# Performance work log

Hardware: AMD Instinct MI355X
Metric: run time of the kernel (lower is better)

The kernel has to match this reference:

```python
import jax, jax.numpy as jnp
import numpy as np

W_DIM, T_DIM = 300, 100
IN = W_DIM + T_DIM        # 400, also LSTM hidden size
H = IN                    # hiddenSize
BI = 2 * H                # 800, biLSTM output per step
MLP_IN = 2 * BI           # 1600
VOCAB, NTAGS = 50000, 50
SEQ = 320


def _lstm_dir(xs, w_ih, w_hh, b_ih, b_hh, h0, c0, reverse):
    # xs: [T, d_in]; PyTorch gate order i, f, g, o
    if reverse:
        xs = xs[::-1]
    def step(carry, x):
        h, c = carry
        g = x @ w_ih.T + h @ w_hh.T + b_ih + b_hh
        i, f, gc, o = jnp.split(g, 4)
        i, f, o = jax.nn.sigmoid(i), jax.nn.sigmoid(f), jax.nn.sigmoid(o)
        c = f * c + i * jnp.tanh(gc)
        h = o * jnp.tanh(c)
        return (h, c), h
    _, ys = jax.lax.scan(step, (h0, c0), xs)
    return ys[::-1] if reverse else ys


def _bilstm(x, params, h0, c0):
    # x: [T, IN]; h0/c0: [4, H] ordered (l0 fwd, l0 bwd, l1 fwd, l1 bwd)
    out = x
    for layer in range(2):
        p_f = params[layer][0]
        p_b = params[layer][1]
        yf = _lstm_dir(out, *p_f, h0[2 * layer],     c0[2 * layer],     False)
        yb = _lstm_dir(out, *p_b, h0[2 * layer + 1], c0[2 * layer + 1], True)
        out = jnp.concatenate([yf, yb], axis=-1)  # [T, 2H]
    return out


def setup_inputs() -> dict:
    key = jax.random.key(0)
    ks = iter(jax.random.split(key, 32))
    inp = {}
    inp['words'] = jax.random.randint(next(ks), (SEQ,), 0, VOCAB)
    inp['tags'] = jax.random.randint(next(ks), (SEQ,), 0, NTAGS)
    inp['arcs'] = jax.random.randint(next(ks), (SEQ + 1,), 0, SEQ + 1)
    inp['word_emb'] = jax.random.normal(next(ks), (VOCAB, W_DIM), jnp.float32) * 0.1
    inp['tag_emb'] = jax.random.normal(next(ks), (NTAGS, T_DIM), jnp.float32) * 0.1
    inp['h0'] = jax.random.normal(next(ks), (4, H), jnp.float32)
    inp['c0'] = jax.random.normal(next(ks), (4, H), jnp.float32)
    s = 1.0 / np.sqrt(H)
    for layer, d_in in ((0, IN), (1, BI)):
        for suf in ('', 'r'):
            inp[f'w_ih_l{layer}{suf}'] = jax.random.uniform(next(ks), (4 * H, d_in), jnp.float32, -s, s)
            inp[f'w_hh_l{layer}{suf}'] = jax.random.uniform(next(ks), (4 * H, H), jnp.float32, -s, s)
            inp[f'b_ih_l{layer}{suf}'] = jax.random.uniform(next(ks), (4 * H,), jnp.float32, -s, s)
            inp[f'b_hh_l{layer}{suf}'] = jax.random.uniform(next(ks), (4 * H,), jnp.float32, -s, s)
    inp['mlp_w1'] = jax.random.normal(next(ks), (MLP_IN, MLP_IN), jnp.float32) * 0.02
    inp['mlp_b1'] = jnp.zeros((MLP_IN,), jnp.float32)
    inp['mlp_w2'] = jax.random.normal(next(ks), (1, MLP_IN), jnp.float32) * 0.02
    inp['mlp_b2'] = jnp.zeros((1,), jnp.float32)
    return inp


def reference(words, tags, arcs, word_emb, tag_emb, h0, c0,
              w_ih_l0, w_hh_l0, b_ih_l0, b_hh_l0,
              w_ih_l0r, w_hh_l0r, b_ih_l0r, b_hh_l0r,
              w_ih_l1, w_hh_l1, b_ih_l1, b_hh_l1,
              w_ih_l1r, w_hh_l1r, b_ih_l1r, b_hh_l1r,
              mlp_w1, mlp_b1, mlp_w2, mlp_b2):
    n = words.shape[0]
    x = jnp.concatenate([word_emb[words], tag_emb[tags]], axis=1)  # [n, IN]
    params = (((w_ih_l0, w_hh_l0, b_ih_l0, b_hh_l0), (w_ih_l0r, w_hh_l0r, b_ih_l0r, b_hh_l0r)),
              ((w_ih_l1, w_hh_l1, b_ih_l1, b_hh_l1), (w_ih_l1r, w_hh_l1r, b_ih_l1r, b_hh_l1r)))
    hv = _bilstm(x, params, h0, c0)  # [n, BI]
    # pairwise MLP: concat(h_head, h_dep) @ W1.T == h_head @ W1a.T + h_dep @ W1b.T
    w1a, w1b = mlp_w1[:, :BI], mlp_w1[:, BI:]
    a = hv @ w1a.T  # [n, MLP_IN], head part
    b = hv @ w1b.T  # [n, MLP_IN], dep part
    hid = jax.nn.relu(a[:, None, :] + b[None, :, :] + mlp_b1)  # [n, n, MLP_IN]
    scores = jnp.einsum('ndk,ok->nd', hid, mlp_w2)[..., 0] if mlp_w2.shape[0] != 1 else (hid @ mlp_w2[0] + mlp_b2[0])  # [n, n]
    offdiag = 1.0 - jnp.eye(n, dtype=scores.dtype)
    score_tensor = jnp.zeros((n + 1, n + 1), scores.dtype)
    score_tensor = score_tensor.at[0, 0].set(1.0)
    score_tensor = score_tensor.at[1:, 1:].set(scores * offdiag)
    return score_tensor
```

## Files before the change

### kernel.cpp

```cpp
#include <hip/hip_runtime.h>
#include <hip/hip_bf16.h>
#include <hip/hip_fp16.h>

#define SEQ   320
#define HDIM  400
#define GATES 1600
#define NCOL  3200
#define GDW   16
#define RPW   25

typedef _Float16 half2v __attribute__((ext_vector_type(2)));
typedef _Float16 f16x8  __attribute__((ext_vector_type(8)));
typedef float    f32x4  __attribute__((ext_vector_type(4)));
union H2U { unsigned u; half2v h; __half2 hh; };

__global__ __launch_bounds__(256) void embed_f16_kernel(
    const int* __restrict__ words, const int* __restrict__ tags,
    const float* __restrict__ wemb, const float* __restrict__ temb,
    _Float16* __restrict__ xh)
{
    int i = blockIdx.x * 256 + threadIdx.x;
    if (i >= SEQ * 416) return;
    int t = i / 416, c = i % 416;
    float v = 0.f;
    if (c < 300)      v = wemb[(size_t)words[t] * 300 + c];
    else if (c < 400) v = temb[(size_t)tags[t] * 100 + (c - 300)];
    xh[i] = (_Float16)v;
}

__global__ __launch_bounds__(256) void cvtB_kernel(
    const float* __restrict__ B0, const float* __restrict__ B1, int ldb,
    int K, int Kp, _Float16* __restrict__ dst)
{
    int i = blockIdx.x * 256 + threadIdx.x;
    if (i >= NCOL * Kp) return;
    int n = i / Kp, k = i % Kp;
    float v = 0.f;
    if (k < K)
        v = (n < GATES) ? B0[(size_t)n * ldb + k] : B1[(size_t)(n - GATES) * ldb + k];
    dst[i] = (_Float16)v;
}

__global__ __launch_bounds__(256) void cvtA_kernel(
    const float* __restrict__ src, _Float16* __restrict__ dst, int n)
{
    int i = blockIdx.x * 256 + threadIdx.x;
    if (i < n) dst[i] = (_Float16)src[i];
}

__global__ __launch_bounds__(256) void bias_kernel(
    const float* __restrict__ bihl0,  const float* __restrict__ bhhl0,
    const float* __restrict__ bihl0r, const float* __restrict__ bhhl0r,
    const float* __restrict__ bihl1,  const float* __restrict__ bhhl1,
    const float* __restrict__ bihl1r, const float* __restrict__ bhhl1r,
    const float* __restrict__ mlpb1,
    float* __restrict__ bL0, float* __restrict__ bL1, float* __restrict__ bAB)
{
    int g = blockIdx.x * 256 + threadIdx.x;
    if (g >= NCOL) return;
    if (g < GATES) {
        bL0[g] = bihl0[g] + bhhl0[g];
        bL1[g] = bihl1[g] + bhhl1[g];
        bAB[g] = mlpb1[g];
    } else {
        int q = g - GATES;
        bL0[g] = bihl0r[q] + bhhl0r[q];
        bL1[g] = bihl1r[q] + bhhl1r[q];
        bAB[g] = 0.f;
    }
}

__global__ __launch_bounds__(256) void gemm_f16(
    const _Float16* __restrict__ A, int Kp,
    const _Float16* __restrict__ B,
    const float* __restrict__ bias, float* __restrict__ C)
{
    const int tid  = threadIdx.x;
    const int w    = tid >> 6, lane = tid & 63;
    const int quad = lane >> 4, l16 = lane & 15;
    const int mb   = blockIdx.y * 32 + (w & 1) * 16;
    const int n0   = blockIdx.x * 64 + (w >> 1) * 32;
    const _Float16* Arow = A + (size_t)(mb + l16) * Kp + quad * 8;
    const _Float16* B0r  = B + (size_t)(n0 + l16) * Kp + quad * 8;
    const _Float16* B1r  = B0r + (size_t)16 * Kp;
    f32x4 acc0 = {0.f, 0.f, 0.f, 0.f}, acc1 = {0.f, 0.f, 0.f, 0.f};
#pragma unroll 4
    for (int k0 = 0; k0 < Kp; k0 += 32) {
        f16x8 a  = *(const f16x8*)(Arow + k0);
        f16x8 b0 = *(const f16x8*)(B0r + k0);
        f16x8 b1 = *(const f16x8*)(B1r + k0);
        acc0 = __builtin_amdgcn_mfma_f32_16x16x32_f16(a, b0, acc0, 0, 0, 0);
        acc1 = __builtin_amdgcn_mfma_f32_16x16x32_f16(a, b1, acc1, 0, 0, 0);
    }
    const int mr = mb + quad * 4;
    float bn0 = bias[n0 + l16], bn1 = bias[n0 + 16 + l16];
#pragma unroll
    for (int r = 0; r < 4; ++r) {
        C[(size_t)(mr + r) * NCOL + n0 + l16]      = acc0[r] + bn0;
        C[(size_t)(mr + r) * NCOL + n0 + 16 + l16] = acc1[r] + bn1;
    }
}

__global__ __launch_bounds__(1024, 4) void lstm_layer(
    const float* __restrict__ gates,
    const float* __restrict__ whh_f, const float* __restrict__ whh_b,
    const float* __restrict__ h0f, const float* __restrict__ h0b,
    const float* __restrict__ c0f, const float* __restrict__ c0b,
    float* out)
{
    __shared__ unsigned h_pk[200];
    __shared__ float part[16][28];
    const int tid = threadIdx.x;
    const int dir = blockIdx.x >> 4;
    const int wg  = blockIdx.x & 15;
    const int j0  = wg * RPW;
    const float* whh = dir ? whh_b : whh_f;
    const float* h0d = dir ? h0b : h0f;
    const float* c0d = dir ? c0b : c0f;

    const int w    = tid >> 6;
    const int lane = tid & 63;
    const int g    = w & 3;
    const int kq   = w >> 2;
    const int half = lane & 1;
    const int r    = lane >> 1;
    const int jrow = j0 + (r < RPW ? r : RPW - 1);

    unsigned wr[26];
    {
        const float2* wp = (const float2*)(whh + (size_t)(g * 400 + jrow) * 400 +
                                           kq * 100 + 48 * half);
#pragma unroll
        for (int i = 0; i < 26; ++i) {
            H2U cv; float2 f = wp[i];
            cv.hh = __floats2half2_rn(f.x, f.y);
            wr[i] = (half == 0 && i >= 24) ? 0u : cv.u;
        }
    }

    const int pc = tid % 100;
    const int pr = tid / 100;
    float c_prev = (tid < RPW) ? c0d[j0 + tid] : 0.f;

    for (int s = 0; s < 320; ++s) {
        const int row = dir ? (319 - s) : s;

        float gv0 = 0.f, gv1 = 0.f, gv2 = 0.f, gv3 = 0.f;
        if (tid < RPW) {
            const float* gx = gates + (size_t)row * NCOL + dir * GATES + j0 + tid;
            gv0 = gx[0]; gv1 = gx[400]; gv2 = gx[800]; gv3 = gx[1200];
        }

        if (s == 0) {
            if (tid < 100) {
                float4 f = ((const float4*)h0d)[tid];
                H2U a, b;
                a.hh = __floats2half2_rn(f.x, f.y);
                b.hh = __floats2half2_rn(f.z, f.w);
                ((uint2*)h_pk)[tid] = make_uint2(a.u, b.u);
            }
        } else if (pr < 4) {
            const int rp = dir ? (row + 1) : (row - 1);
            const unsigned long long* src =
                (const unsigned long long*)(out + (size_t)rp * 800 + dir * 400) + pc * 2;
            unsigned long long a, b;
            for (;;) {
                a = __hip_atomic_load(src,     __ATOMIC_RELAXED, __HIP_MEMORY_SCOPE_AGENT);
                b = __hip_atomic_load(src + 1, __ATOMIC_RELAXED, __HIP_MEMORY_SCOPE_AGENT);
                if ((unsigned)a != 0xFFFFFFFFu && (unsigned)(a >> 32) != 0xFFFFFFFFu &&
                    (unsigned)b != 0xFFFFFFFFu && (unsigned)(b >> 32) != 0xFFFFFFFFu)
                    break;
            }
            H2U p0, p1;
            p0.hh = __floats2half2_rn(__uint_as_float((unsigned)a),
                                      __uint_as_float((unsigned)(a >> 32)));
            p1.hh = __floats2half2_rn(__uint_as_float((unsigned)b),
                                      __uint_as_float((unsigned)(b >> 32)));
            ((uint2*)h_pk)[pc] = make_uint2(p0.u, p1.u);
        }
        __syncthreads();

        {
            const uint2* hp2 = (const uint2*)h_pk + kq * 25 + 12 * half;
            float acc = 0.f;
#pragma unroll
            for (int i = 0; i < 13; ++i) {
                uint2 hv = hp2[i];
                H2U w0, w1, x0, x1;
                w0.u = wr[2 * i]; w1.u = wr[2 * i + 1];
                x0.u = hv.x;      x1.u = hv.y;
                acc = __builtin_amdgcn_fdot2(w0.h, x0.h, acc, false);
                acc = __builtin_amdgcn_fdot2(w1.h, x1.h, acc, false);
            }
            acc += __shfl_xor(acc, 1, 64);
            if (half == 0 && r < RPW) part[w][r] = acc;
        }
        __syncthreads();

        if (tid < RPW) {
            float gi = gv0 + ((part[0][tid] + part[4][tid]) + (part[8][tid]  + part[12][tid]));
            float gf = gv1 + ((part[1][tid] + part[5][tid]) + (part[9][tid]  + part[13][tid]));
            float gg = gv2 + ((part[2][tid] + part[6][tid]) + (part[10][tid] + part[14][tid]));
            float go = gv3 + ((part[3][tid] + part[7][tid]) + (part[11][tid] + part[15][tid]));
            float iv = 1.f / (1.f + __expf(-gi));
            float fv = 1.f / (1.f + __expf(-gf));
            float ov = 1.f / (1.f + __expf(-go));
            float tg = 1.f - 2.f / (1.f + __expf(2.f * gg));
            c_prev = fv * c_prev + iv * tg;
            float tc = 1.f - 2.f / (1.f + __expf(2.f * c_prev));
            float hv = ov * tc;
            __hip_atomic_store((unsigned*)(out + (size_t)row * 800 + dir * 400 + j0 + tid),
                               __float_as_uint(hv), __ATOMIC_RELAXED,
                               __HIP_MEMORY_SCOPE_AGENT);
        }
    }
}

__global__ __launch_bounds__(256) void scores_kernel(
    const float* __restrict__ ab, const float* __restrict__ w2,
    const float* __restrict__ b2, float* __restrict__ out)
{
    __shared__ float a_s[16 * 132];
    __shared__ float b_s[16 * 132];
    __shared__ float w_s[128];
    const int tx = threadIdx.x, ty = threadIdx.y;
    const int tid = ty * 16 + tx;
    const int n0 = blockIdx.y * 16, d0 = blockIdx.x * 16;
    float acc = 0.f;
    for (int kc = 0; kc < 1600; kc += 128) {
        for (int i = tid; i < 16 * 128; i += 256) {
            int r = i >> 7, c = i & 127;
            a_s[r * 132 + c] = ab[(size_t)(n0 + r) * NCOL + kc + c];
            b_s[r * 132 + c] = ab[(size_t)(d0 + r) * NCOL + 1600 + kc + c];
        }
        if (tid < 128) w_s[tid] = w2[kc + tid];
        __syncthreads();
#pragma unroll
        for (int k = 0; k < 128; k += 4) {
            float4 av = *(const float4*)&a_s[ty * 132 + k];
            float4 bv = *(const float4*)&b_s[tx * 132 + k];
            float4 wv = *(const float4*)&w_s[k];
            acc += fmaxf(av.x + bv.x, 0.f) * wv.x;
            acc += fmaxf(av.y + bv.y, 0.f) * wv.y;
            acc += fmaxf(av.z + bv.z, 0.f) * wv.z;
            acc += fmaxf(av.w + bv.w, 0.f) * wv.w;
        }
        __syncthreads();
    }
    int n = n0 + ty, d = d0 + tx;
    out[(size_t)(n + 1) * 321 + (d + 1)] = (n == d) ? 0.f : (acc + b2[0]);
}

__global__ void border_kernel(float* out) {
    int i = blockIdx.x * 256 + threadIdx.x;
    if (i < 321) {
        out[i]               = (i == 0) ? 1.f : 0.f;
        out[(size_t)i * 321] = (i == 0) ? 1.f : 0.f;
    }
}

extern "C" void kernel_launch(void* const* d_in, const int* in_sizes, int n_in,
                              void* d_out, int out_size, void* d_ws, size_t ws_size,
                              hipStream_t stream)
{
    const int*   words    = (const int*)d_in[0];
    const int*   tags     = (const int*)d_in[1];
    const float* wemb     = (const float*)d_in[3];
    const float* temb     = (const float*)d_in[4];
    const float* h0       = (const float*)d_in[5];
    const float* c0       = (const float*)d_in[6];
    const float* w_ih_l0  = (const float*)d_in[7];
    const float* w_hh_l0  = (const float*)d_in[8];
    const float* b_ih_l0  = (const float*)d_in[9];
    const float* b_hh_l0  = (const float*)d_in[10];
    const float* w_ih_l0r = (const float*)d_in[11];
    const float* w_hh_l0r = (const float*)d_in[12];
    const float* b_ih_l0r = (const float*)d_in[13];
    const float* b_hh_l0r = (const float*)d_in[14];
    const float* w_ih_l1  = (const float*)d_in[15];
    const float* w_hh_l1  = (const float*)d_in[16];
    const float* b_ih_l1  = (const float*)d_in[17];
    const float* b_hh_l1  = (const float*)d_in[18];
    const float* w_ih_l1r = (const float*)d_in[19];
    const float* w_hh_l1r = (const float*)d_in[20];
    const float* b_ih_l1r = (const float*)d_in[21];
    const float* b_hh_l1r = (const float*)d_in[22];
    const float* mlp_w1   = (const float*)d_in[23];
    const float* mlp_b1   = (const float*)d_in[24];
    const float* mlp_w2   = (const float*)d_in[25];
    const float* mlp_b2   = (const float*)d_in[26];
    float* out = (float*)d_out;

    float* ws     = (float*)d_ws;
    float* out0   = ws + 128000;
    float* out1   = ws + 384000;
    float* gates  = ws + 640000;
    float* biasL0 = ws + 1664000;
    float* biasL1 = ws + 1667200;
    float* biasAB = ws + 1670400;
    _Float16* Ah  = (_Float16*)(ws + 1673600);
    _Float16* Bh  = (_Float16*)(ws + 1801600);

    hipMemsetAsync(out0, 0xFF, (size_t)2 * 256000 * 4, stream);

    embed_f16_kernel<<<520, 256, 0, stream>>>(words, tags, wemb, temb, Ah);
    bias_kernel<<<13, 256, 0, stream>>>(b_ih_l0, b_hh_l0, b_ih_l0r, b_hh_l0r,
                                        b_ih_l1, b_hh_l1, b_ih_l1r, b_hh_l1r,
                                        mlp_b1, biasL0, biasL1, biasAB);

    cvtB_kernel<<<(NCOL * 416 + 255) / 256, 256, 0, stream>>>(
        w_ih_l0, w_ih_l0r, 400, 400, 416, Bh);
    gemm_f16<<<dim3(50, 10), 256, 0, stream>>>(Ah, 416, Bh, biasL0, gates);
    lstm_layer<<<2 * GDW, 1024, 0, stream>>>(gates, w_hh_l0, w_hh_l0r,
                                             h0, h0 + 400, c0, c0 + 400, out0);

    cvtA_kernel<<<1000, 256, 0, stream>>>(out0, Ah, 256000);
    cvtB_kernel<<<(NCOL * 800 + 255) / 256, 256, 0, stream>>>(
        w_ih_l1, w_ih_l1r, 800, 800, 800, Bh);
    gemm_f16<<<dim3(50, 10), 256, 0, stream>>>(Ah, 800, Bh, biasL1, gates);
    lstm_layer<<<2 * GDW, 1024, 0, stream>>>(gates, w_hh_l1, w_hh_l1r,
                                             h0 + 800, h0 + 1200, c0 + 800, c0 + 1200,
                                             out1);

    cvtA_kernel<<<1000, 256, 0, stream>>>(out1, Ah, 256000);
    cvtB_kernel<<<(NCOL * 800 + 255) / 256, 256, 0, stream>>>(
        mlp_w1, mlp_w1 + 800, 1600, 800, 800, Bh);
    gemm_f16<<<dim3(50, 10), 256, 0, stream>>>(Ah, 800, Bh, biasAB, gates);

    dim3 sgrid(20, 20), sblock(16, 16);
    scores_kernel<<<sgrid, sblock, 0, stream>>>(gates, mlp_w2, mlp_b2, out);
    border_kernel<<<2, 256, 0, stream>>>(out);
}
```

Baseline: 1.582 ms.

## Exchange packed fp16 hidden state between LSTM workgroups and fuse prep kernels

```diff
diff --git a/kernel.cpp b/kernel.cpp
--- a/kernel.cpp
+++ b/kernel.cpp
@@ -3,7 +3,6 @@
 #include <hip/hip_fp16.h>
 
 #define SEQ   320
-#define HDIM  400
 #define GATES 1600
 #define NCOL  3200
 #define GDW   16
@@ -14,59 +13,71 @@
 typedef float    f32x4  __attribute__((ext_vector_type(4)));
 union H2U { unsigned u; half2v h; __half2 hh; };
 
-__global__ __launch_bounds__(256) void embed_f16_kernel(
+__global__ __launch_bounds__(256) void prep_kernel(
     const int* __restrict__ words, const int* __restrict__ tags,
     const float* __restrict__ wemb, const float* __restrict__ temb,
-    _Float16* __restrict__ xh)
-{
-    int i = blockIdx.x * 256 + threadIdx.x;
-    if (i >= SEQ * 416) return;
-    int t = i / 416, c = i % 416;
-    float v = 0.f;
-    if (c < 300)      v = wemb[(size_t)words[t] * 300 + c];
-    else if (c < 400) v = temb[(size_t)tags[t] * 100 + (c - 300)];
-    xh[i] = (_Float16)v;
-}
-
-__global__ __launch_bounds__(256) void cvtB_kernel(
-    const float* __restrict__ B0, const float* __restrict__ B1, int ldb,
-    int K, int Kp, _Float16* __restrict__ dst)
-{
-    int i = blockIdx.x * 256 + threadIdx.x;
-    if (i >= NCOL * Kp) return;
-    int n = i / Kp, k = i % Kp;
-    float v = 0.f;
-    if (k < K)
-        v = (n < GATES) ? B0[(size_t)n * ldb + k] : B1[(size_t)(n - GATES) * ldb + k];
-    dst[i] = (_Float16)v;
-}
-
-__global__ __launch_bounds__(256) void cvtA_kernel(
-    const float* __restrict__ src, _Float16* __restrict__ dst, int n)
-{
-    int i = blockIdx.x * 256 + threadIdx.x;
-    if (i < n) dst[i] = (_Float16)src[i];
-}
-
-__global__ __launch_bounds__(256) void bias_kernel(
+    _Float16* __restrict__ Ah0,
     const float* __restrict__ bihl0,  const float* __restrict__ bhhl0,
     const float* __restrict__ bihl0r, const float* __restrict__ bhhl0r,
     const float* __restrict__ bihl1,  const float* __restrict__ bhhl1,
     const float* __restrict__ bihl1r, const float* __restrict__ bhhl1r,
     const float* __restrict__ mlpb1,
-    float* __restrict__ bL0, float* __restrict__ bL1, float* __restrict__ bAB)
-{
-    int g = blockIdx.x * 256 + threadIdx.x;
-    if (g >= NCOL) return;
-    if (g < GATES) {
-        bL0[g] = bihl0[g] + bhhl0[g];
-        bL1[g] = bihl1[g] + bhhl1[g];
-        bAB[g] = mlpb1[g];
+    float* __restrict__ bL0, float* __restrict__ bL1, float* __restrict__ bAB,
+    const float* __restrict__ wih0, const float* __restrict__ wih0r,
+    _Float16* __restrict__ BhA)
+{
+    const int b = blockIdx.x, t = threadIdx.x;
+    if (b < 520) {
+        int i = b * 256 + t;
+        if (i >= SEQ * 416) return;
+        int tt = i / 416, c = i % 416;
+        float v = 0.f;
+        if (c < 300)      v = wemb[(size_t)words[tt] * 300 + c];
+        else if (c < 400) v = temb[(size_t)tags[tt] * 100 + (c - 300)];
+        Ah0[i] = (_Float16)v;
+    } else if (b < 533) {
+        int g = (b - 520) * 256 + t;
+        if (g >= NCOL) return;
+        if (g < GATES) {
+            bL0[g] = bihl0[g] + bhhl0[g];
+            bL1[g] = bihl1[g] + bhhl1[g];
+            bAB[g] = mlpb1[g];
+        } else {
+            int q = g - GATES;
+            bL0[g] = bihl0r[q] + bhhl0r[q];
+            bL1[g] = bihl1r[q] + bhhl1r[q];
+            bAB[g] = 0.f;
+        }
     } else {
-        int q = g - GATES;
-        bL0[g] = bihl0r[q] + bhhl0r[q];
-        bL1[g] = bihl1r[q] + bhhl1r[q];
-        bAB[g] = 0.f;
+        int i = (b - 533) * 256 + t;
+        if (i >= NCOL * 416) return;
+        int n = i / 416, k = i % 416;
+        float v = 0.f;
+        if (k < 400)
+            v = (n < GATES) ? wih0[(size_t)n * 400 + k]
+                            : wih0r[(size_t)(n - GATES) * 400 + k];
+        BhA[i] = (_Float16)v;
+    }
+}
+
+__global__ __launch_bounds__(256) void cvt2_kernel(
+    const float* __restrict__ wih1, const float* __restrict__ wih1r,
+    _Float16* __restrict__ BhB,
+    const float* __restrict__ mlpw1, _Float16* __restrict__ BhA)
+{
+    const int b = blockIdx.x, t = threadIdx.x;
+    if (b < 10000) {
+        int i = b * 256 + t;
+        if (i >= NCOL * 800) return;
+        int n = i / 800, k = i % 800;
+        BhB[i] = (_Float16)((n < GATES) ? wih1[(size_t)n * 800 + k]
+                                        : wih1r[(size_t)(n - GATES) * 800 + k]);
+    } else {
+        int i = (b - 10000) * 256 + t;
+        if (i >= NCOL * 800) return;
+        int n = i / 800, k = i % 800;
+        BhA[i] = (_Float16)((n < GATES) ? mlpw1[(size_t)n * 1600 + k]
+                                        : mlpw1[(size_t)(n - GATES) * 1600 + 800 + k]);
     }
 }
 
@@ -106,10 +117,12 @@
     const float* __restrict__ whh_f, const float* __restrict__ whh_b,
     const float* __restrict__ h0f, const float* __restrict__ h0b,
     const float* __restrict__ c0f, const float* __restrict__ c0b,
-    float* out)
+    unsigned* __restrict__ ex,
+    _Float16* __restrict__ ah)
 {
     __shared__ unsigned h_pk[200];
     __shared__ float part[16][28];
+    unsigned short* hs = (unsigned short*)h_pk;
     const int tid = threadIdx.x;
     const int dir = blockIdx.x >> 4;
     const int wg  = blockIdx.x & 15;
@@ -138,8 +151,8 @@
         }
     }
 
-    const int pc = tid % 100;
-    const int pr = tid / 100;
+    const int pp = tid / 13;
+    const int pd = tid - pp * 13;
     float c_prev = (tid < RPW) ? c0d[j0 + tid] : 0.f;
 
     for (int s = 0; s < 320; ++s) {
@@ -159,24 +172,18 @@
                 b.hh = __floats2half2_rn(f.z, f.w);
                 ((uint2*)h_pk)[tid] = make_uint2(a.u, b.u);
             }
-        } else if (pr < 4) {
+        } else if (tid < 208 && pp != wg) {
             const int rp = dir ? (row + 1) : (row - 1);
-            const unsigned long long* src =
-                (const unsigned long long*)(out + (size_t)rp * 800 + dir * 400) + pc * 2;
-            unsigned long long a, b;
+            const unsigned* src = ex + (((size_t)dir * GDW + pp) * SEQ + rp) * 16 + pd;
+            unsigned v;
             for (;;) {
-                a = __hip_atomic_load(src,     __ATOMIC_RELAXED, __HIP_MEMORY_SCOPE_AGENT);
-                b = __hip_atomic_load(src + 1, __ATOMIC_RELAXED, __HIP_MEMORY_SCOPE_AGENT);
-                if ((unsigned)a != 0xFFFFFFFFu && (unsigned)(a >> 32) != 0xFFFFFFFFu &&
-                    (unsigned)b != 0xFFFFFFFFu && (unsigned)(b >> 32) != 0xFFFFFFFFu)
-                    break;
-            }
-            H2U p0, p1;
-            p0.hh = __floats2half2_rn(__uint_as_float((unsigned)a),
-                                      __uint_as_float((unsigned)(a >> 32)));
-            p1.hh = __floats2half2_rn(__uint_as_float((unsigned)b),
-                                      __uint_as_float((unsigned)(b >> 32)));
-            ((uint2*)h_pk)[pc] = make_uint2(p0.u, p1.u);
+                v = __hip_atomic_load(src, __ATOMIC_RELAXED, __HIP_MEMORY_SCOPE_AGENT);
+                if ((v & 0xFFFFu) != 0xFFFFu &&
+                    (pd == 12 || (v >> 16) != 0xFFFFu)) break;
+            }
+            const int hb = pp * RPW + pd * 2;
+            hs[hb] = (unsigned short)(v & 0xFFFFu);
+            if (pd < 12) hs[hb + 1] = (unsigned short)(v >> 16);
         }
         __syncthreads();
 
@@ -185,10 +192,10 @@
             float acc = 0.f;
 #pragma unroll
             for (int i = 0; i < 13; ++i) {
-                uint2 hv = hp2[i];
+                uint2 hv2 = hp2[i];
                 H2U w0, w1, x0, x1;
                 w0.u = wr[2 * i]; w1.u = wr[2 * i + 1];
-                x0.u = hv.x;      x1.u = hv.y;
+                x0.u = hv2.x;     x1.u = hv2.y;
                 acc = __builtin_amdgcn_fdot2(w0.h, x0.h, acc, false);
                 acc = __builtin_amdgcn_fdot2(w1.h, x1.h, acc, false);
             }
@@ -197,6 +204,7 @@
         }
         __syncthreads();
 
+        float hv = 0.f;
         if (tid < RPW) {
             float gi = gv0 + ((part[0][tid] + part[4][tid]) + (part[8][tid]  + part[12][tid]));
             float gf = gv1 + ((part[1][tid] + part[5][tid]) + (part[9][tid]  + part[13][tid]));
@@ -208,10 +216,24 @@
             float tg = 1.f - 2.f / (1.f + __expf(2.f * gg));
             c_prev = fv * c_prev + iv * tg;
             float tc = 1.f - 2.f / (1.f + __expf(2.f * c_prev));
-            float hv = ov * tc;
-            __hip_atomic_store((unsigned*)(out + (size_t)row * 800 + dir * 400 + j0 + tid),
-                               __float_as_uint(hv), __ATOMIC_RELAXED,
-                               __HIP_MEMORY_SCOPE_AGENT);
+            hv = ov * tc;
+        }
+        if (w == 0) {
+            int i0 = 2 * lane     < 63 ? 2 * lane     : 63;
+            int i1 = 2 * lane + 1 < 63 ? 2 * lane + 1 : 63;
+            float xlo = __shfl(hv, i0, 64);
+            float xhi = __shfl(hv, i1, 64);
+            if (lane < 13) {
+                H2U pk;
+                pk.hh = __floats2half2_rn(xlo, (2 * lane + 1 < RPW) ? xhi : 0.f);
+                __hip_atomic_store(ex + (((size_t)dir * GDW + wg) * SEQ + row) * 16 + lane,
+                                   pk.u, __ATOMIC_RELAXED, __HIP_MEMORY_SCOPE_AGENT);
+            }
+            if (tid < RPW) {
+                ah[(size_t)row * 800 + dir * 400 + j0 + tid] = (_Float16)hv;
+                H2U o; o.hh = __floats2half2_rn(hv, 0.f);
+                hs[RPW * wg + tid] = (unsigned short)(o.u & 0xFFFFu);
+            }
         }
     }
 }
@@ -220,6 +242,14 @@
     const float* __restrict__ ab, const float* __restrict__ w2,
     const float* __restrict__ b2, float* __restrict__ out)
 {
+    if (blockIdx.y == 20) {
+        int i = blockIdx.x * 256 + threadIdx.y * 16 + threadIdx.x;
+        if (blockIdx.x < 2 && i < 321) {
+            out[i]               = (i == 0) ? 1.f : 0.f;
+            out[(size_t)i * 321] = (i == 0) ? 1.f : 0.f;
+        }
+        return;
+    }
     __shared__ float a_s[16 * 132];
     __shared__ float b_s[16 * 132];
     __shared__ float w_s[128];
@@ -249,14 +279,6 @@
     }
     int n = n0 + ty, d = d0 + tx;
     out[(size_t)(n + 1) * 321 + (d + 1)] = (n == d) ? 0.f : (acc + b2[0]);
-}
-
-__global__ void border_kernel(float* out) {
-    int i = blockIdx.x * 256 + threadIdx.x;
-    if (i < 321) {
-        out[i]               = (i == 0) ? 1.f : 0.f;
-        out[(size_t)i * 321] = (i == 0) ? 1.f : 0.f;
-    }
 }
 
 extern "C" void kernel_launch(void* const* d_in, const int* in_sizes, int n_in,
@@ -291,43 +313,36 @@
     const float* mlp_b2   = (const float*)d_in[26];
     float* out = (float*)d_out;
 
-    float* ws     = (float*)d_ws;
-    float* out0   = ws + 128000;
-    float* out1   = ws + 384000;
-    float* gates  = ws + 640000;
-    float* biasL0 = ws + 1664000;
-    float* biasL1 = ws + 1667200;
-    float* biasAB = ws + 1670400;
-    _Float16* Ah  = (_Float16*)(ws + 1673600);
-    _Float16* Bh  = (_Float16*)(ws + 1801600);
-
-    hipMemsetAsync(out0, 0xFF, (size_t)2 * 256000 * 4, stream);
-
-    embed_f16_kernel<<<520, 256, 0, stream>>>(words, tags, wemb, temb, Ah);
-    bias_kernel<<<13, 256, 0, stream>>>(b_ih_l0, b_hh_l0, b_ih_l0r, b_hh_l0r,
-                                        b_ih_l1, b_hh_l1, b_ih_l1r, b_hh_l1r,
-                                        mlp_b1, biasL0, biasL1, biasAB);
-
-    cvtB_kernel<<<(NCOL * 416 + 255) / 256, 256, 0, stream>>>(
-        w_ih_l0, w_ih_l0r, 400, 400, 416, Bh);
-    gemm_f16<<<dim3(50, 10), 256, 0, stream>>>(Ah, 416, Bh, biasL0, gates);
+    float* ws      = (float*)d_ws;
+    float*    gates  = ws;
+    float*    biasL0 = ws + 1024000;
+    float*    biasL1 = ws + 1027200;
+    float*    biasAB = ws + 1030400;
+    unsigned* ex     = (unsigned*)(ws + 1033600);
+    _Float16* Ah0    = (_Float16*)(ws + 1361280);
+    _Float16* Ah1    = (_Float16*)(ws + 1427840);
+    _Float16* Ah2    = (_Float16*)(ws + 1555840);
+    _Float16* BhA    = (_Float16*)(ws + 1683840);
+    _Float16* BhB    = (_Float16*)(ws + 2963840);
+    unsigned* ex0 = ex, *ex1 = ex + 163840;
+
+    hipMemsetAsync(ex, 0xFF, 327680u * 4, stream);
+
+    prep_kernel<<<5733, 256, 0, stream>>>(
+        words, tags, wemb, temb, Ah0,
+        b_ih_l0, b_hh_l0, b_ih_l0r, b_hh_l0r,
+        b_ih_l1, b_hh_l1, b_ih_l1r, b_hh_l1r,
+        mlp_b1, biasL0, biasL1, biasAB, w_ih_l0, w_ih_l0r, BhA);
+
+    gemm_f16<<<dim3(50, 10), 256, 0, stream>>>(Ah0, 416, BhA, biasL0, gates);
+    cvt2_kernel<<<20000, 256, 0, stream>>>(w_ih_l1, w_ih_l1r, BhB, mlp_w1, BhA);
     lstm_layer<<<2 * GDW, 1024, 0, stream>>>(gates, w_hh_l0, w_hh_l0r,
-                                             h0, h0 + 400, c0, c0 + 400, out0);
-
-    cvtA_kernel<<<1000, 256, 0, stream>>>(out0, Ah, 256000);
-    cvtB_kernel<<<(NCOL * 800 + 255) / 256, 256, 0, stream>>>(
-        w_ih_l1, w_ih_l1r, 800, 800, 800, Bh);
-    gemm_f16<<<dim3(50, 10), 256, 0, stream>>>(Ah, 800, Bh, biasL1, gates);
+                                             h0, h0 + 400, c0, c0 + 400, ex0, Ah1);
+    gemm_f16<<<dim3(50, 10), 256, 0, stream>>>(Ah1, 800, BhB, biasL1, gates);
     lstm_layer<<<2 * GDW, 1024, 0, stream>>>(gates, w_hh_l1, w_hh_l1r,
                                              h0 + 800, h0 + 1200, c0 + 800, c0 + 1200,
-                                             out1);
-
-    cvtA_kernel<<<1000, 256, 0, stream>>>(out1, Ah, 256000);
-    cvtB_kernel<<<(NCOL * 800 + 255) / 256, 256, 0, stream>>>(
-        mlp_w1, mlp_w1 + 800, 1600, 800, 800, Bh);
-    gemm_f16<<<dim3(50, 10), 256, 0, stream>>>(Ah, 800, Bh, biasAB, gates);
-
-    dim3 sgrid(20, 20), sblock(16, 16);
-    scores_kernel<<<sgrid, sblock, 0, stream>>>(gates, mlp_w2, mlp_b2, out);
-    border_kernel<<<2, 256, 0, stream>>>(out);
-}
+                                             ex1, Ah2);
+    gemm_f16<<<dim3(50, 10), 256, 0, stream>>>(Ah2, 800, BhA, biasAB, gates);
+
+    scores_kernel<<<dim3(20, 21), dim3(16, 16), 0, stream>>>(gates, mlp_w2, mlp_b2, out);
+}
```

New measurement: 1.357 ms. 1.17x faster.
